# Kernel optimization log

Hardware: AMD Instinct MI355X
Metric: run time of the kernel (lower is better)

## Reference

```python
import jax, jax.numpy as jnp
import numpy as np


def setup_inputs() -> dict:
    key = jax.random.key(0)
    k1, k2 = jax.random.split(key)
    B, M, QT, KVT, H = 4, 16, 1024, 1024, 64
    s = jax.random.normal(k1, (B, M, QT, KVT), dtype=jnp.float32)
    v = jax.random.normal(k2, (B, M, KVT, H), dtype=jnp.float32)
    return {"s": s, "v": v}


def reference(s, v):
    # Original: broadcast-multiply [B,M,QT,KVT,H] then sum over KVT.
    # Mathematically a batched matmul: out[b,m,q,h] = sum_k s[b,m,q,k] * v[b,m,k,h]
    return jnp.einsum('bmqk,bmkh->bmqh', s, v)
```

## Files before the change

### kernel.cpp

```cpp
#include <hip/hip_runtime.h>
#include <stdint.h>


typedef __bf16 bf16x8 __attribute__((ext_vector_type(8)));
typedef float  f32x4  __attribute__((ext_vector_type(4)));

#define QTDIM 1024
#define KVDIM 1024
#define HDIM  64
#define QTILE 128
#define BK    64
#define NK    (KVDIM / BK)
#define SSTR  72
#define THREADS 256

__device__ __forceinline__ uint32_t pack_bf16_2(float lo, float hi) {
    union { float f; uint32_t u; } a, b;
    a.f = lo; b.f = hi;
    return __builtin_amdgcn_perm(b.u, a.u, 0x07060302u);
}

__global__ __launch_bounds__(THREADS, 2) void svbmm_kernel(
    const float* __restrict__ s, const float* __restrict__ v, float* __restrict__ out)
{
    __shared__ uint16_t s_sm[QTILE * SSTR];
    __shared__ uint16_t vt_sm[HDIM * SSTR];

    const int tid = threadIdx.x;
    const int bm  = blockIdx.y;
    const int q0  = blockIdx.x * QTILE;

    const float* sp = s   + ((size_t)bm * QTDIM + q0) * (size_t)KVDIM;
    const float* vp = v   + (size_t)bm * KVDIM * HDIM;
    float*       op = out + ((size_t)bm * QTDIM + q0) * (size_t)HDIM;

    const int srow = tid >> 4;
    const int scol = (tid & 15) << 2;
    const int vh   = tid & 63;
    const int vk0  = (tid >> 6) << 4;

    float4 sreg[8];
    float  vreg[16];

    {
        const float* sb = sp + srow * KVDIM + scol;
        #pragma unroll
        for (int i = 0; i < 8; ++i)
            sreg[i] = *(const float4*)(sb + i * 16 * KVDIM);
        const float* vb = vp + vk0 * HDIM + vh;
        #pragma unroll
        for (int j = 0; j < 16; ++j)
            vreg[j] = vb[j * HDIM];
    }

    f32x4 acc[2][4];
    #pragma unroll
    for (int mt = 0; mt < 2; ++mt)
        #pragma unroll
        for (int nt = 0; nt < 4; ++nt)
            acc[mt][nt] = (f32x4){0.f, 0.f, 0.f, 0.f};

    const int wave = tid >> 6;
    const int lane = tid & 63;
    const int lrow = lane & 15;
    const int quad = lane >> 4;

    #pragma unroll 1
    for (int kt = 0; kt < NK; ++kt) {
        #pragma unroll
        for (int i = 0; i < 8; ++i) {
            float4 f = sreg[i];
            uint32_t u01 = pack_bf16_2(f.x, f.y);
            uint32_t u23 = pack_bf16_2(f.z, f.w);
            uint32_t* dst = (uint32_t*)&s_sm[(srow + i * 16) * SSTR + scol];
            dst[0] = u01;
            dst[1] = u23;
        }
        #pragma unroll
        for (int p = 0; p < 8; ++p) {
            uint32_t u = pack_bf16_2(vreg[2 * p], vreg[2 * p + 1]);
            *(uint32_t*)&vt_sm[vh * SSTR + vk0 + 2 * p] = u;
        }
        __syncthreads();

        if (kt + 1 < NK) {
            const float* sb = sp + srow * KVDIM + (kt + 1) * BK + scol;
            #pragma unroll
            for (int i = 0; i < 8; ++i)
                sreg[i] = *(const float4*)(sb + i * 16 * KVDIM);
            const float* vb = vp + ((kt + 1) * BK + vk0) * HDIM + vh;
            #pragma unroll
            for (int j = 0; j < 16; ++j)
                vreg[j] = vb[j * HDIM];
        }

        #pragma unroll
        for (int kk = 0; kk < 2; ++kk) {
            const int col = kk * 32 + quad * 8;
            bf16x8 a[2], b[4];
            #pragma unroll
            for (int mt = 0; mt < 2; ++mt)
                a[mt] = *(const bf16x8*)&s_sm[(wave * 32 + mt * 16 + lrow) * SSTR + col];
            #pragma unroll
            for (int nt = 0; nt < 4; ++nt)
                b[nt] = *(const bf16x8*)&vt_sm[(nt * 16 + lrow) * SSTR + col];
            #pragma unroll
            for (int mt = 0; mt < 2; ++mt)
                #pragma unroll
                for (int nt = 0; nt < 4; ++nt)
                    acc[mt][nt] = __builtin_amdgcn_mfma_f32_16x16x32_bf16(
                        a[mt], b[nt], acc[mt][nt], 0, 0, 0);
        }
        __syncthreads();
    }

    #pragma unroll
    for (int mt = 0; mt < 2; ++mt) {
        #pragma unroll
        for (int nt = 0; nt < 4; ++nt) {
            #pragma unroll
            for (int r = 0; r < 4; ++r) {
                const int row = wave * 32 + mt * 16 + quad * 4 + r;
                const int col = nt * 16 + lrow;
                op[row * HDIM + col] = acc[mt][nt][r];
            }
        }
    }
}

extern "C" void kernel_launch(void* const* d_in, const int* in_sizes, int n_in,
                              void* d_out, int out_size, void* d_ws, size_t ws_size,
                              hipStream_t stream) {
    const float* s = (const float*)d_in[0];
    const float* v = (const float*)d_in[1];
    float* out = (float*)d_out;
    const int BM = in_sizes[0] / (QTDIM * KVDIM);
    dim3 grid(QTDIM / QTILE, BM);
    svbmm_kernel<<<grid, THREADS, 0, stream>>>(s, v, out);
}
```

Before: 391.9 us.

## Halve Q tile, double-buffer LDS and drop trailing barrier

Reduces the Q tile from 128 to 64 rows so each wave computes a single 16-row MFMA tile, which doubles the grid and raises the occupancy target to 4 blocks per CU. Shared-memory tiles are double-buffered so the second __syncthreads per iteration can be removed, and LDS stores are widened to 64-bit. The aim is better latency hiding on this memory-bound fp32 load stream. In exchange, V is now loaded and converted twice as often per output row, and MFMA work per LDS read drops.

```diff
diff --git a/kernel.cpp b/kernel.cpp
--- a/kernel.cpp
+++ b/kernel.cpp
@@ -8,7 +8,7 @@
 #define QTDIM 1024
 #define KVDIM 1024
 #define HDIM  64
-#define QTILE 128
+#define QTILE 64
 #define BK    64
 #define NK    (KVDIM / BK)
 #define SSTR  72
@@ -20,11 +20,11 @@
     return __builtin_amdgcn_perm(b.u, a.u, 0x07060302u);
 }
 
-__global__ __launch_bounds__(THREADS, 2) void svbmm_kernel(
+__global__ __launch_bounds__(THREADS, 4) void svbmm_kernel(
     const float* __restrict__ s, const float* __restrict__ v, float* __restrict__ out)
 {
-    __shared__ uint16_t s_sm[QTILE * SSTR];
-    __shared__ uint16_t vt_sm[HDIM * SSTR];
+    __shared__ uint16_t s_sm[2][QTILE * SSTR];
+    __shared__ uint16_t vt_sm[2][HDIM * SSTR];
 
     const int tid = threadIdx.x;
     const int bm  = blockIdx.y;
@@ -39,13 +39,13 @@
     const int vh   = tid & 63;
     const int vk0  = (tid >> 6) << 4;
 
-    float4 sreg[8];
+    float4 sreg[4];
     float  vreg[16];
 
     {
         const float* sb = sp + srow * KVDIM + scol;
         #pragma unroll
-        for (int i = 0; i < 8; ++i)
+        for (int i = 0; i < 4; ++i)
             sreg[i] = *(const float4*)(sb + i * 16 * KVDIM);
         const float* vb = vp + vk0 * HDIM + vh;
         #pragma unroll
@@ -53,40 +53,40 @@
             vreg[j] = vb[j * HDIM];
     }
 
-    f32x4 acc[2][4];
+    f32x4 acc[4];
     #pragma unroll
-    for (int mt = 0; mt < 2; ++mt)
-        #pragma unroll
-        for (int nt = 0; nt < 4; ++nt)
-            acc[mt][nt] = (f32x4){0.f, 0.f, 0.f, 0.f};
+    for (int nt = 0; nt < 4; ++nt)
+        acc[nt] = (f32x4){0.f, 0.f, 0.f, 0.f};
 
     const int wave = tid >> 6;
     const int lane = tid & 63;
     const int lrow = lane & 15;
     const int quad = lane >> 4;
 
-    #pragma unroll 1
+    #pragma unroll 2
     for (int kt = 0; kt < NK; ++kt) {
+        const int buf = kt & 1;
+
         #pragma unroll
-        for (int i = 0; i < 8; ++i) {
+        for (int i = 0; i < 4; ++i) {
             float4 f = sreg[i];
-            uint32_t u01 = pack_bf16_2(f.x, f.y);
-            uint32_t u23 = pack_bf16_2(f.z, f.w);
-            uint32_t* dst = (uint32_t*)&s_sm[(srow + i * 16) * SSTR + scol];
-            dst[0] = u01;
-            dst[1] = u23;
+            uint64_t u = (uint64_t)pack_bf16_2(f.x, f.y)
+                       | ((uint64_t)pack_bf16_2(f.z, f.w) << 32);
+            *(uint64_t*)&s_sm[buf][(srow + i * 16) * SSTR + scol] = u;
         }
         #pragma unroll
-        for (int p = 0; p < 8; ++p) {
-            uint32_t u = pack_bf16_2(vreg[2 * p], vreg[2 * p + 1]);
-            *(uint32_t*)&vt_sm[vh * SSTR + vk0 + 2 * p] = u;
+        for (int p = 0; p < 4; ++p) {
+            uint64_t u = (uint64_t)pack_bf16_2(vreg[4 * p],     vreg[4 * p + 1])
+                       | ((uint64_t)pack_bf16_2(vreg[4 * p + 2], vreg[4 * p + 3]) << 32);
+            *(uint64_t*)&vt_sm[buf][vh * SSTR + vk0 + 4 * p] = u;
         }
+
         __syncthreads();
 
         if (kt + 1 < NK) {
             const float* sb = sp + srow * KVDIM + (kt + 1) * BK + scol;
             #pragma unroll
-            for (int i = 0; i < 8; ++i)
+            for (int i = 0; i < 4; ++i)
                 sreg[i] = *(const float4*)(sb + i * 16 * KVDIM);
             const float* vb = vp + ((kt + 1) * BK + vk0) * HDIM + vh;
             #pragma unroll
@@ -97,33 +97,22 @@
         #pragma unroll
         for (int kk = 0; kk < 2; ++kk) {
             const int col = kk * 32 + quad * 8;
-            bf16x8 a[2], b[4];
+            bf16x8 a = *(const bf16x8*)&s_sm[buf][(wave * 16 + lrow) * SSTR + col];
             #pragma unroll
-            for (int mt = 0; mt < 2; ++mt)
-                a[mt] = *(const bf16x8*)&s_sm[(wave * 32 + mt * 16 + lrow) * SSTR + col];
-            #pragma unroll
-            for (int nt = 0; nt < 4; ++nt)
-                b[nt] = *(const bf16x8*)&vt_sm[(nt * 16 + lrow) * SSTR + col];
-            #pragma unroll
-            for (int mt = 0; mt < 2; ++mt)
-                #pragma unroll
-                for (int nt = 0; nt < 4; ++nt)
-                    acc[mt][nt] = __builtin_amdgcn_mfma_f32_16x16x32_bf16(
-                        a[mt], b[nt], acc[mt][nt], 0, 0, 0);
+            for (int nt = 0; nt < 4; ++nt) {
+                bf16x8 b = *(const bf16x8*)&vt_sm[buf][(nt * 16 + lrow) * SSTR + col];
+                acc[nt] = __builtin_amdgcn_mfma_f32_16x16x32_bf16(a, b, acc[nt], 0, 0, 0);
+            }
         }
-        __syncthreads();
     }
 
     #pragma unroll
-    for (int mt = 0; mt < 2; ++mt) {
+    for (int nt = 0; nt < 4; ++nt) {
         #pragma unroll
-        for (int nt = 0; nt < 4; ++nt) {
-            #pragma unroll
-            for (int r = 0; r < 4; ++r) {
-                const int row = wave * 32 + mt * 16 + quad * 4 + r;
-                const int col = nt * 16 + lrow;
-                op[row * HDIM + col] = acc[mt][nt][r];
-            }
+        for (int r = 0; r < 4; ++r) {
+            const int row = wave * 16 + quad * 4 + r;
+            const int col = nt * 16 + lrow;
+            op[row * HDIM + col] = acc[nt][r];
         }
     }
 }
```

Measured after the change: 381.6 us. 2.6% less time.
